# Kernel tuning notes

Measured on AMD Instinct MI355X. Metric: run time of the kernel, lower is better.

Reference implementation:

```python
import jax, jax.numpy as jnp
import numpy as np

B, N, D_MODEL, ATT_DIM, H = 2, 2048, 1024, 1024, 8
HEAD_DIM = ATT_DIM // H


def setup_inputs() -> dict:
    key = jax.random.key(0)
    ks = jax.random.split(key, 10)
    s_in = 1.0 / np.sqrt(D_MODEL)
    s_att = 1.0 / np.sqrt(ATT_DIM)
    x = jax.random.normal(ks[0], (B, N, D_MODEL), dtype=jnp.float32)
    mask = jax.random.randint(ks[1], (B, 1, N, N), 0, 2) == 1
    Wq = jax.random.uniform(ks[2], (D_MODEL, ATT_DIM), jnp.float32, -s_in, s_in)
    bq = jnp.zeros((ATT_DIM,), jnp.float32)
    Wk = jax.random.uniform(ks[3], (D_MODEL, ATT_DIM), jnp.float32, -s_in, s_in)
    bk = jnp.zeros((ATT_DIM,), jnp.float32)
    Wv = jax.random.uniform(ks[4], (D_MODEL, ATT_DIM), jnp.float32, -s_in, s_in)
    bv = jnp.zeros((ATT_DIM,), jnp.float32)
    Wo = jax.random.uniform(ks[5], (ATT_DIM, D_MODEL), jnp.float32, -s_att, s_att)
    bo = jnp.zeros((D_MODEL,), jnp.float32)
    return {"x": x, "mask": mask, "Wq": Wq, "bq": bq, "Wk": Wk, "bk": bk,
            "Wv": Wv, "bv": bv, "Wo": Wo, "bo": bo}


def reference(x, mask, Wq, bq, Wk, bk, Wv, bv, Wo, bo):
    # x: [B, N, d_model]; dropout is identity (eval mode) for a deterministic baseline.
    b, n, d_model = x.shape
    scale = d_model ** (-0.5)  # NOTE: original scales by d_model, not head_dim

    def split_heads(t):  # [B, N, att] -> [B, H, N, head]
        return t.reshape(b, n, H, HEAD_DIM).transpose(0, 2, 1, 3)

    q = split_heads(x @ Wq + bq)
    k = split_heads(x @ Wk + bk)
    v = split_heads(x @ Wv + bv)
    score = jnp.einsum('bhqd,bhkd->bhqk', q, k) * scale
    score = jnp.where(mask, -jnp.inf, score)
    w = jax.nn.softmax(score, axis=-1)
    out = jnp.einsum('bhqk,bhkd->bhqd', w, v)            # [B, H, N, head]
    out = out.transpose(0, 2, 1, 3).reshape(b, n, ATT_DIM)
    return out @ Wo + bo
```

## Files before the change

kernel.cpp:

```cpp
#include <hip/hip_runtime.h>
#include <stdint.h>

typedef __bf16 bf16_t;
typedef bf16_t bf16x8 __attribute__((ext_vector_type(8)));
typedef float f32x4 __attribute__((ext_vector_type(4)));
typedef float f32x16 __attribute__((ext_vector_type(16)));
typedef unsigned int u32;
typedef unsigned long long u64;

#define B_ 2
#define N_ 2048
#define DM 1024
#define H_ 8
#define HD 128

#define GLDS16(g, l) __builtin_amdgcn_global_load_lds(                      \
    (const __attribute__((address_space(1))) void*)(g),                     \
    (__attribute__((address_space(3))) void*)(l), 16, 0, 0)

__global__ void cvt_kernel(const float* __restrict__ in, bf16_t* __restrict__ out, int n8)
{
    int i = blockIdx.x * blockDim.x + threadIdx.x;
    if (i >= n8) return;
    const float4 a = *(const float4*)(in + (size_t)i * 8);
    const float4 b = *(const float4*)(in + (size_t)i * 8 + 4);
    bf16x8 o;
    o[0] = (bf16_t)a.x; o[1] = (bf16_t)a.y; o[2] = (bf16_t)a.z; o[3] = (bf16_t)a.w;
    o[4] = (bf16_t)b.x; o[5] = (bf16_t)b.y; o[6] = (bf16_t)b.z; o[7] = (bf16_t)b.w;
    *(bf16x8*)(out + (size_t)i * 8) = o;
}

__global__ void transpose_cvt4(const float* __restrict__ Wq, const float* __restrict__ Wk,
                               const float* __restrict__ Wv, const float* __restrict__ Wo,
                               bf16_t* __restrict__ Wqkvt, bf16_t* __restrict__ Wot)
{
    __shared__ float t[32][33];
    const int z = blockIdx.z;
    const float* W = (z == 0) ? Wq : (z == 1) ? Wk : (z == 2) ? Wv : Wo;
    bf16_t* Wt = (z < 3) ? (Wqkvt + (size_t)z * DM * DM) : Wot;
    const int tx = threadIdx.x & 31;
    const int ty = threadIdx.x >> 5;
    const int bx = blockIdx.x * 32;
    const int by = blockIdx.y * 32;
#pragma unroll
    for (int i = 0; i < 32; i += 8)
        t[ty + i][tx] = W[(size_t)(by + ty + i) * 1024 + bx + tx];
    __syncthreads();
#pragma unroll
    for (int i = 0; i < 32; i += 8)
        Wt[(size_t)(bx + ty + i) * 1024 + by + tx] = (bf16_t)t[tx][ty + i];
}

__global__ void mask_pack(const int* __restrict__ mask, u64* __restrict__ mb, int nwords)
{
    const int t = blockIdx.x * blockDim.x + threadIdx.x;
    const int w = t >> 6;
    if (w >= nwords) return;
    const int v = mask[(size_t)w * 64 + (t & 63)];
    const u64 bits = __ballot(v != 0);
    if ((t & 63) == 0) mb[w] = bits;
}

template<int MODE>
__global__ __launch_bounds__(256)
void gemm_bt(const bf16_t* __restrict__ A, const bf16_t* __restrict__ Bt,
             const float* __restrict__ b0, const float* __restrict__ b1,
             const float* __restrict__ b2,
             void* __restrict__ Cout, bf16_t* __restrict__ VtOut,
             const int M, const int N, const int K, const int ldc, const int gy)
{
    __shared__ bf16_t sA[2][128 * 32];
    __shared__ bf16_t sB[2][128 * 32];

    const int tid  = threadIdx.x;
    const int wv   = tid >> 6;
    const int lane = tid & 63;
    const int fr   = lane & 15;
    const int fk   = (lane >> 4) * 8;

    const int nwg = gridDim.x;
    const int swz = ((int)blockIdx.x & 7) * (nwg >> 3) + ((int)blockIdx.x >> 3);
    const int by  = swz % gy;
    const int bx  = swz / gy;

    const int row0 = bx * 128;
    const int col0 = by * 128;
    const int wr   = (wv >> 1) * 64;
    const int wc   = (wv & 1) * 64;

    const int srow = wv * 32 + (lane >> 2);
    const int scol = (lane & 3) * 8;

    const bf16_t* gA0 = A  + (size_t)(row0 + srow) * K + scol;
    const bf16_t* gA1 = gA0 + (size_t)16 * K;
    const bf16_t* gB0 = Bt + (size_t)(col0 + srow) * K + scol;
    const bf16_t* gB1 = gB0 + (size_t)16 * K;

    const int ldst0 = wv * 1024;
    const int ldst1 = wv * 1024 + 512;

    f32x4 acc[4][4] = {};
    const int NT = K >> 5;

    GLDS16(gA0, &sA[0][ldst0]);
    GLDS16(gA1, &sA[0][ldst1]);
    GLDS16(gB0, &sB[0][ldst0]);
    GLDS16(gB1, &sB[0][ldst1]);
    __syncthreads();

    for (int kt = 0; kt < NT; ++kt) {
        const int cur = kt & 1;
        if (kt + 1 < NT) {
            const size_t ko = (size_t)(kt + 1) * 32;
            GLDS16(gA0 + ko, &sA[cur ^ 1][ldst0]);
            GLDS16(gA1 + ko, &sA[cur ^ 1][ldst1]);
            GLDS16(gB0 + ko, &sB[cur ^ 1][ldst0]);
            GLDS16(gB1 + ko, &sB[cur ^ 1][ldst1]);
        }
        bf16x8 af[4], bfr[4];
#pragma unroll
        for (int i = 0; i < 4; ++i)
            af[i] = *(const bf16x8*)&sA[cur][(wr + i * 16 + fr) * 32 + fk];
#pragma unroll
        for (int i = 0; i < 4; ++i)
            bfr[i] = *(const bf16x8*)&sB[cur][(wc + i * 16 + fr) * 32 + fk];
#pragma unroll
        for (int i = 0; i < 4; ++i)
#pragma unroll
            for (int j = 0; j < 4; ++j)
                acc[i][j] = __builtin_amdgcn_mfma_f32_16x16x32_bf16(af[i], bfr[j], acc[i][j], 0, 0, 0);
        __syncthreads();
    }

#pragma unroll
    for (int i = 0; i < 4; ++i) {
#pragma unroll
        for (int j = 0; j < 4; ++j) {
            const int c = col0 + wc + j * 16 + fr;
            const int seg = c >> 10;
            const float bb = (seg == 0) ? b0[c] : (seg == 1 ? b1[c - 1024] : b2[c - 2048]);
#pragma unroll
            for (int r = 0; r < 4; ++r) {
                const int row = row0 + wr + i * 16 + (lane >> 4) * 4 + r;
                const float v = acc[i][j][r] + bb;
                if constexpr (MODE == 1) {
                    ((float*)Cout)[(size_t)row * ldc + c] = v;
                } else if constexpr (MODE == 0) {
                    ((bf16_t*)Cout)[(size_t)row * ldc + c] = (bf16_t)v;
                } else {
                    if (c < 2048) {
                        ((bf16_t*)Cout)[(size_t)row * ldc + c] = (bf16_t)v;
                    } else {
                        const int ch = c - 2048;
                        const int bb_ = row >> 11;
                        const int nn  = row & 2047;
                        VtOut[((size_t)(bb_ * H_ + (ch >> 7)) * HD + (ch & 127)) * N_ + nn] = (bf16_t)v;
                    }
                }
            }
        }
    }
}

__device__ __forceinline__ u32 pk2(float lo, float hi)
{
    union { bf16_t h[2]; u32 u; } t;
    t.h[0] = (bf16_t)lo; t.h[1] = (bf16_t)hi;
    return t.u;
}

__global__ __launch_bounds__(256, 2)
void flash_attn(const bf16_t* __restrict__ QK, const bf16_t* __restrict__ Vt,
                const u64* __restrict__ mbits, bf16_t* __restrict__ On,
                float* __restrict__ Ls)
{
    __shared__ bf16_t sK[2][64 * 128];
    __shared__ bf16_t sVt[2][128 * 64];

    const int tid  = threadIdx.x;
    const int wv   = tid >> 6;
    const int lane = tid & 63;
    const int lq   = lane & 31;
    const int hi   = lane >> 5;
    const int g4   = lane >> 4;
    const int fr   = lane & 15;

    const int wid = ((int)blockIdx.x & 7) * 64 + ((int)blockIdx.x >> 3);
    const int s   = wid >> 8;
    const int bh  = (wid >> 4) & 15;
    const int qb  = wid & 15;
    const int b   = bh >> 3;
    const int h   = bh & 7;
    const int q0  = qb * 128;
    const int kvbase = s * 1024;

    const int q = q0 + wv * 32 + lq;
    const size_t qoff = ((size_t)(b * N_ + q)) * 2048 + h * HD + hi * 8;
    bf16x8 qf[8];
#pragma unroll
    for (int kk = 0; kk < 8; ++kk) {
        bf16x8 t = *(const bf16x8*)&QK[qoff + kk * 16];
#pragma unroll
        for (int e = 0; e < 8; ++e) qf[kk][e] = (bf16_t)((float)t[e] * 0.04508422f);
    }

    const bf16_t* kg[4]; int kdo[4];
#pragma unroll
    for (int n = 0; n < 4; ++n) {
        const int row = wv * 16 + n * 4 + g4;
        kg[n] = QK + ((size_t)(b * N_ + kvbase + row)) * 2048 + 1024 + h * HD
                   + ((fr * 8) ^ ((row & 15) << 3));
        kdo[n] = (wv * 16 + n * 4) * 128;
    }
    const bf16_t* vg[4]; int vdo[4];
    {
        const int l8 = lane >> 3;
        const int c8 = (lane & 7) * 8;
#pragma unroll
        for (int n = 0; n < 4; ++n) {
            const int d = wv * 32 + n * 8 + l8;
            vg[n] = Vt + ((size_t)((b * H_ + h) * HD + d)) * N_ + kvbase + (c8 ^ (l8 << 3));
            vdo[n] = (wv * 32 + n * 8) * 64;
        }
    }
    const size_t mrow = ((size_t)(b * N_ + q)) * 32 + s * 16;

    f32x16 acc_o[4] = {};
    float lsum = 0.0f;

    const int ksw = (lq & 15) << 3;
    const int vsw = (lq & 7) << 3;

#pragma unroll
    for (int n = 0; n < 4; ++n) {
        GLDS16(kg[n], &sK[0][kdo[n]]);
        GLDS16(vg[n], &sVt[0][vdo[n]]);
    }

    for (int kc = 0; kc < 16; ++kc) {
        const int cur = kc & 1;
        __syncthreads();

        if (kc + 1 < 16) {
#pragma unroll
            for (int n = 0; n < 4; ++n) {
                GLDS16(kg[n] + (size_t)(kc + 1) * 64 * 2048, &sK[cur ^ 1][kdo[n]]);
                GLDS16(vg[n] + (kc + 1) * 64, &sVt[cur ^ 1][vdo[n]]);
            }
        }
        const u64 mb = mbits[mrow + kc];

        f32x16 st0 = {}, st1 = {};
#pragma unroll
        for (int kk = 0; kk < 8; ++kk) {
            const int co = (kk * 16 + hi * 8) ^ ksw;
            bf16x8 kb0 = *(const bf16x8*)&sK[cur][lq * 128 + co];
            bf16x8 kb1 = *(const bf16x8*)&sK[cur][(32 + lq) * 128 + co];
            st0 = __builtin_amdgcn_mfma_f32_32x32x16_bf16(kb0, qf[kk], st0, 0, 0, 0);
            st1 = __builtin_amdgcn_mfma_f32_32x32x16_bf16(kb1, qf[kk], st1, 0, 0, 0);
        }

        bf16x8 paf[4];
#pragma unroll
        for (int t32 = 0; t32 < 2; ++t32) {
            float p[16];
#pragma unroll
            for (int r = 0; r < 16; ++r) {
                const int kv = t32 * 32 + (r & 3) + 8 * (r >> 2) + 4 * hi;
                const float e = exp2f(t32 ? st1[r] : st0[r]);
                p[r] = ((mb >> kv) & 1ull) ? 0.0f : e;
                lsum += p[r];
            }
            u32 w0 = pk2(p[0], p[1]),   w1 = pk2(p[2], p[3]);
            u32 w2 = pk2(p[4], p[5]),   w3 = pk2(p[6], p[7]);
            u32 w4 = pk2(p[8], p[9]),   w5 = pk2(p[10], p[11]);
            u32 w6 = pk2(p[12], p[13]), w7 = pk2(p[14], p[15]);
            asm volatile("v_permlane32_swap_b32 %0, %1" : "+v"(w0), "+v"(w2));
            asm volatile("v_permlane32_swap_b32 %0, %1" : "+v"(w1), "+v"(w3));
            asm volatile("v_permlane32_swap_b32 %0, %1" : "+v"(w4), "+v"(w6));
            asm volatile("v_permlane32_swap_b32 %0, %1" : "+v"(w5), "+v"(w7));
            union { u32 u[4]; bf16x8 v; } f0, f1;
            f0.u[0] = w0; f0.u[1] = w1; f0.u[2] = w2; f0.u[3] = w3;
            f1.u[0] = w4; f1.u[1] = w5; f1.u[2] = w6; f1.u[3] = w7;
            paf[t32 * 2]     = f0.v;
            paf[t32 * 2 + 1] = f1.v;
        }

#pragma unroll
        for (int dt = 0; dt < 4; ++dt) {
            const int vr = (dt * 32 + lq) * 64;
#pragma unroll
            for (int ks = 0; ks < 4; ++ks) {
                bf16x8 vb = *(const bf16x8*)&sVt[cur][vr + ((ks * 16 + hi * 8) ^ vsw)];
                acc_o[dt] = __builtin_amdgcn_mfma_f32_32x32x16_bf16(paf[ks], vb, acc_o[dt], 0, 0, 0);
            }
        }
    }

    lsum += __shfl_xor(lsum, 32, 64);

#pragma unroll
    for (int dt = 0; dt < 4; ++dt) {
#pragma unroll
        for (int r = 0; r < 16; ++r) {
            const int qg = q0 + wv * 32 + (r & 3) + 8 * (r >> 2) + 4 * hi;
            On[((size_t)(s * 4096 + b * N_ + qg)) * 1024 + h * HD + dt * 32 + lq] =
                (bf16_t)acc_o[dt][r];
        }
    }
    if (lane < 32)
        Ls[((size_t)((s * 2 + b) * 8 + h)) * 2048 + q0 + wv * 32 + lane] = lsum;
}

__global__ void combine(const bf16_t* __restrict__ On, const float* __restrict__ Ls,
                        bf16_t* __restrict__ AO)
{
    const int idx = blockIdx.x * 256 + threadIdx.x;
    const int row = idx >> 7;
    const int c8  = (idx & 127) * 8;
    const int b = row >> 11;
    const int n = row & 2047;
    const int h = c8 >> 7;
    const float l0 = Ls[((size_t)(b * 8 + h)) * 2048 + n];
    const float l1 = Ls[((size_t)((2 + b) * 8 + h)) * 2048 + n];
    const float w  = 1.0f / (l0 + l1);
    bf16x8 a = *(const bf16x8*)&On[(size_t)row * 1024 + c8];
    bf16x8 d = *(const bf16x8*)&On[(size_t)4096 * 1024 + (size_t)row * 1024 + c8];
    bf16x8 o;
#pragma unroll
    for (int e = 0; e < 8; ++e)
        o[e] = (bf16_t)(((float)a[e] + (float)d[e]) * w);
    *(bf16x8*)&AO[(size_t)row * 1024 + c8] = o;
}

extern "C" void kernel_launch(void* const* d_in, const int* in_sizes, int n_in,
                              void* d_out, int out_size, void* d_ws, size_t ws_size,
                              hipStream_t stream)
{
    const float* x  = (const float*)d_in[0];
    const int* mask = (const int*)d_in[1];
    const float* Wq = (const float*)d_in[2];
    const float* bq = (const float*)d_in[3];
    const float* Wk = (const float*)d_in[4];
    const float* bk = (const float*)d_in[5];
    const float* Wv = (const float*)d_in[6];
    const float* bv = (const float*)d_in[7];
    const float* Wo = (const float*)d_in[8];
    const float* bo = (const float*)d_in[9];
    float* out = (float*)d_out;

    const size_t MT = (size_t)B_ * N_;
    const size_t M1 = 1024 * 1024;
    bf16_t* wsb   = (bf16_t*)d_ws;
    bf16_t* On    = wsb;
    bf16_t* xb    = wsb;
    bf16_t* Wqkvt = wsb + 4 * M1;
    bf16_t* Wot   = wsb + 8 * M1;
    bf16_t* QKb   = wsb + 9 * M1;
    bf16_t* Vtb   = QKb + MT * 2048;
    bf16_t* AOb   = Vtb + (size_t)B_ * H_ * HD * N_;
    u64*    mbits = (u64*)(AOb + MT * DM);
    float*  Ls    = (float*)(mbits + (size_t)B_ * N_ * 32);

    cvt_kernel<<<2048, 256, 0, stream>>>(x, xb, (int)(MT * DM / 8));

    transpose_cvt4<<<dim3(32, 32, 4), 256, 0, stream>>>(Wq, Wk, Wv, Wo, Wqkvt, Wot);

    const int nwords = B_ * N_ * (N_ / 64);
    mask_pack<<<nwords / 4, 256, 0, stream>>>(mask, mbits, nwords);

    gemm_bt<2><<<768, 256, 0, stream>>>(
        xb, Wqkvt, bq, bk, bv, QKb, Vtb, (int)MT, 3072, DM, 2048, 24);

    flash_attn<<<512, 256, 0, stream>>>(QKb, Vtb, mbits, On, Ls);

    combine<<<2048, 256, 0, stream>>>(On, Ls, AOb);

    gemm_bt<1><<<256, 256, 0, stream>>>(
        AOb, Wot, bo, bo, bo, out, nullptr, (int)MT, DM, DM, DM, 8);
}
```

Measured before the change: 248.6 us.

## Single-buffer V tile via register staging to fit three blocks per CU

V tiles are no longer double-buffered in LDS through direct global-to-LDS loads. Each chunk is prefetched into registers and written into a single LDS buffer at the top of every iteration, which lowers shared memory use so launch bounds can request three blocks per CU. The mask word is also prefetched one iteration ahead, and the row-sum accumulation is split into four partial sums to shorten the dependency chain. The cost is an extra barrier per iteration, more VGPR pressure from the staged V registers, and possible spills under the tighter occupancy bound.

```diff
diff --git a/kernel.cpp b/kernel.cpp
--- a/kernel.cpp
+++ b/kernel.cpp
@@ -169,13 +169,13 @@
     return t.u;
 }
 
-__global__ __launch_bounds__(256, 2)
+__global__ __launch_bounds__(256, 3)
 void flash_attn(const bf16_t* __restrict__ QK, const bf16_t* __restrict__ Vt,
                 const u64* __restrict__ mbits, bf16_t* __restrict__ On,
                 float* __restrict__ Ls)
 {
     __shared__ bf16_t sK[2][64 * 128];
-    __shared__ bf16_t sVt[2][128 * 64];
+    __shared__ bf16_t sVt[128 * 64];
 
     const int tid  = threadIdx.x;
     const int wv   = tid >> 6;
@@ -212,43 +212,47 @@
                    + ((fr * 8) ^ ((row & 15) << 3));
         kdo[n] = (wv * 16 + n * 4) * 128;
     }
-    const bf16_t* vg[4]; int vdo[4];
-    {
-        const int l8 = lane >> 3;
-        const int c8 = (lane & 7) * 8;
-#pragma unroll
-        for (int n = 0; n < 4; ++n) {
-            const int d = wv * 32 + n * 8 + l8;
-            vg[n] = Vt + ((size_t)((b * H_ + h) * HD + d)) * N_ + kvbase + (c8 ^ (l8 << 3));
-            vdo[n] = (wv * 32 + n * 8) * 64;
-        }
+    const bf16_t* vsrc[4]; int vdoff[4];
+#pragma unroll
+    for (int rr = 0; rr < 4; ++rr) {
+        const int ch = rr * 256 + tid;
+        const int d  = ch >> 3;
+        const int nc = (ch & 7) * 8;
+        vsrc[rr]  = Vt + ((size_t)((b * H_ + h) * HD + d)) * N_ + kvbase + nc;
+        vdoff[rr] = d * 64 + (nc ^ ((d & 7) << 3));
     }
     const size_t mrow = ((size_t)(b * N_ + q)) * 32 + s * 16;
 
     f32x16 acc_o[4] = {};
-    float lsum = 0.0f;
+    float lsp[4] = {0.f, 0.f, 0.f, 0.f};
 
     const int ksw = (lq & 15) << 3;
     const int vsw = (lq & 7) << 3;
 
-#pragma unroll
-    for (int n = 0; n < 4; ++n) {
-        GLDS16(kg[n], &sK[0][kdo[n]]);
-        GLDS16(vg[n], &sVt[0][vdo[n]]);
-    }
+    bf16x8 vst[4];
+#pragma unroll
+    for (int n = 0; n < 4; ++n) GLDS16(kg[n], &sK[0][kdo[n]]);
+#pragma unroll
+    for (int rr = 0; rr < 4; ++rr) vst[rr] = *(const bf16x8*)&vsrc[rr][0];
+    u64 mb_cur = mbits[mrow];
 
     for (int kc = 0; kc < 16; ++kc) {
         const int cur = kc & 1;
+
+#pragma unroll
+        for (int rr = 0; rr < 4; ++rr) *(bf16x8*)&sVt[vdoff[rr]] = vst[rr];
         __syncthreads();
 
+        u64 mb_next = 0;
         if (kc + 1 < 16) {
 #pragma unroll
-            for (int n = 0; n < 4; ++n) {
+            for (int n = 0; n < 4; ++n)
                 GLDS16(kg[n] + (size_t)(kc + 1) * 64 * 2048, &sK[cur ^ 1][kdo[n]]);
-                GLDS16(vg[n] + (kc + 1) * 64, &sVt[cur ^ 1][vdo[n]]);
-            }
-        }
-        const u64 mb = mbits[mrow + kc];
+#pragma unroll
+            for (int rr = 0; rr < 4; ++rr)
+                vst[rr] = *(const bf16x8*)&vsrc[rr][(kc + 1) * 64];
+            mb_next = mbits[mrow + kc + 1];
+        }
 
         f32x16 st0 = {}, st1 = {};
 #pragma unroll
@@ -268,8 +272,8 @@
             for (int r = 0; r < 16; ++r) {
                 const int kv = t32 * 32 + (r & 3) + 8 * (r >> 2) + 4 * hi;
                 const float e = exp2f(t32 ? st1[r] : st0[r]);
-                p[r] = ((mb >> kv) & 1ull) ? 0.0f : e;
-                lsum += p[r];
+                p[r] = ((mb_cur >> kv) & 1ull) ? 0.0f : e;
+                lsp[r & 3] += p[r];
             }
             u32 w0 = pk2(p[0], p[1]),   w1 = pk2(p[2], p[3]);
             u32 w2 = pk2(p[4], p[5]),   w3 = pk2(p[6], p[7]);
@@ -285,18 +289,21 @@
             paf[t32 * 2]     = f0.v;
             paf[t32 * 2 + 1] = f1.v;
         }
+        mb_cur = mb_next;
 
 #pragma unroll
         for (int dt = 0; dt < 4; ++dt) {
             const int vr = (dt * 32 + lq) * 64;
 #pragma unroll
             for (int ks = 0; ks < 4; ++ks) {
-                bf16x8 vb = *(const bf16x8*)&sVt[cur][vr + ((ks * 16 + hi * 8) ^ vsw)];
+                bf16x8 vb = *(const bf16x8*)&sVt[vr + ((ks * 16 + hi * 8) ^ vsw)];
                 acc_o[dt] = __builtin_amdgcn_mfma_f32_32x32x16_bf16(paf[ks], vb, acc_o[dt], 0, 0, 0);
             }
         }
-    }
-
+        __syncthreads();
+    }
+
+    float lsum = (lsp[0] + lsp[1]) + (lsp[2] + lsp[3]);
     lsum += __shfl_xor(lsum, 32, 64);
 
 #pragma unroll
```

New measurement: 520.5 us. +109.3%, slower.
